# Optimization experiments

Hardware: AMD Instinct MI355X
Metric: run time of the kernel (lower is better)

## Reference

```python
import jax, jax.numpy as jnp
import numpy as np

B, S, D = 2, 2048, 2048
H, DH, DR = 16, 128, 64
DC_KV, DC_Q = 512, 1536
ROPE_BASE = 10000.0


def _rope(t):
    """Apply rotate-half RoPE over the last dim of t: [B, S, H, DR]."""
    s, dr = t.shape[1], t.shape[-1]
    inv_freq = 1.0 / (ROPE_BASE ** (jnp.arange(0, dr, 2, dtype=jnp.float32) / dr))
    ang = jnp.arange(s, dtype=jnp.float32)[:, None] * inv_freq  # [S, DR/2]
    cos = jnp.tile(jnp.cos(ang), (1, 2))[None, :, None, :]  # [1,S,1,DR]
    sin = jnp.tile(jnp.sin(ang), (1, 2))[None, :, None, :]
    t1, t2 = jnp.split(t, 2, axis=-1)
    rot = jnp.concatenate([-t2, t1], axis=-1)
    return t * cos + rot * sin


def setup_inputs() -> dict:
    key = jax.random.key(0)
    ks = jax.random.split(key, 18)
    g = lambda k, shp: (jax.random.normal(k, shp, dtype=jnp.float32) * 0.02)
    return {
        "x": jax.random.normal(ks[0], (B, S, D), dtype=jnp.float32),
        "Wkd": g(ks[1], (DC_KV, D)),   "bkd": jnp.zeros((DC_KV,), jnp.float32),
        "Wqd": g(ks[2], (DC_Q, D)),    "bqd": jnp.zeros((DC_Q,), jnp.float32),
        "Wku": g(ks[3], (H * DH, DC_KV)), "bku": jnp.zeros((H * DH,), jnp.float32),
        "Wvu": g(ks[4], (H * DH, DC_KV)), "bvu": jnp.zeros((H * DH,), jnp.float32),
        "Wqu": g(ks[5], (H * DH, DC_Q)),  "bqu": jnp.zeros((H * DH,), jnp.float32),
        "Wkr": g(ks[6], (H * DR, D)),     "bkr": jnp.zeros((H * DR,), jnp.float32),
        "Wqr": g(ks[7], (H * DR, DC_Q)),  "bqr": jnp.zeros((H * DR,), jnp.float32),
        "Wo": g(ks[8], (D, H * DH)),      "bo": jnp.zeros((D,), jnp.float32),
    }


def reference(x, Wkd, bkd, Wqd, bqd, Wku, bku, Wvu, bvu, Wqu, bqu,
              Wkr, bkr, Wqr, bqr, Wo, bo):
    b, s, _ = x.shape
    # 1. Compress to latent spaces
    kv_c = x @ Wkd.T + bkd          # [B,S,DC_KV]
    q_c = x @ Wqd.T + bqd           # [B,S,DC_Q]
    # 2-3. Up-project content / value / rope features
    k_cnt = (kv_c @ Wku.T + bku).reshape(b, s, H, DH)
    v = (kv_c @ Wvu.T + bvu).reshape(b, s, H, DH)
    q_cnt = (q_c @ Wqu.T + bqu).reshape(b, s, H, DH)
    k_r = (x @ Wkr.T + bkr).reshape(b, s, H, DR)      # keys rope from input (eq. 3)
    q_r = (q_c @ Wqr.T + bqr).reshape(b, s, H, DR)    # query rope from latent (eq. 8)
    # 5. Partial RoPE: rotate position features, concat with content
    q_full = jnp.concatenate([q_cnt, _rope(q_r)], axis=-1)  # [B,S,H,DH+DR]
    k_full = jnp.concatenate([k_cnt, _rope(k_r)], axis=-1)
    # 7. Manual causal attention (mscale = 1)
    scale = 1.0 / jnp.sqrt(jnp.float32(DH + DR))
    scores = jnp.einsum("bqhd,bkhd->bhqk", q_full, k_full) * scale
    causal = jnp.tril(jnp.ones((s, s), dtype=bool))
    scores = jnp.where(causal[None, None], scores, jnp.float32(-1e9))
    probs = jax.nn.softmax(scores, axis=-1)
    attn = jnp.einsum("bhqk,bkhd->bqhd", probs, v).reshape(b, s, H * DH)
    # 9. Output projection
    return attn @ Wo.T + bo
```

## Files before the change

### kernel.cpp

```cpp
#include <hip/hip_runtime.h>
#include <stdint.h>
#include <stddef.h>

#define BB 2
#define SS 2048
#define DD 2048
#define HH 16
#define DHH 128
#define DRR 64
#define DCKV 512
#define DCQ 1536

typedef __attribute__((ext_vector_type(8))) short short8;
typedef __attribute__((ext_vector_type(4))) short short4v;
typedef __attribute__((ext_vector_type(4))) float f32x4;
typedef unsigned int u32;

__device__ __forceinline__ short f2bf(float x) {
  unsigned u = __float_as_uint(x);
  u += 0x7fffu + ((u >> 16) & 1u);
  return (short)(u >> 16);
}
__device__ __forceinline__ float bf2f(short s) {
  return __uint_as_float(((unsigned)(unsigned short)s) << 16);
}

__device__ __forceinline__ void gl2lds16(const short* g, short* l) {
  __builtin_amdgcn_global_load_lds(
      (const __attribute__((address_space(1))) u32*)g,
      (__attribute__((address_space(3))) u32*)l, 16, 0, 0);
}

__global__ __launch_bounds__(256) void cast_bf16_kernel(const float* __restrict__ in,
                                                        short* __restrict__ out, int n4) {
  int i = blockIdx.x * 256 + threadIdx.x;
  if (i >= n4) return;
  f32x4 f = ((const f32x4*)in)[i];
  short4v o;
  o[0] = f2bf(f[0]); o[1] = f2bf(f[1]); o[2] = f2bf(f[2]); o[3] = f2bf(f[3]);
  ((short4v*)out)[i] = o;
}

__global__ __launch_bounds__(256) void concat_bias_kernel(
    const float* bkd, const float* bqd, const float* bkr,
    const float* bqu, const float* bqr, const float* bku, const float* bvu,
    float* cb1, float* cb2, float* cb3) {
  int idx = blockIdx.x * 256 + threadIdx.x;
  if (idx < 3072) {
    cb1[idx] = idx < 512 ? bkd[idx] : (idx < 2048 ? bqd[idx - 512] : bkr[idx - 2048]);
  } else if (idx < 6144) {
    int j = idx - 3072;
    cb2[j] = j < 2048 ? bqu[j] : bqr[j - 2048];
  } else if (idx < 10240) {
    int j = idx - 6144;
    cb3[j] = j < 2048 ? bku[j] : bvu[j - 2048];
  }
}

template<int MODE>
__global__ __launch_bounds__(256) void gemm_bt(const short* __restrict__ A, int lda,
                                               const short* __restrict__ Bm, int ldb,
                                               const float* __restrict__ bias,
                                               void* __restrict__ Cout, void* __restrict__ out2,
                                               int M, int N, int K) {
  __shared__ __align__(16) short sA[128 * 32];
  __shared__ __align__(16) short sB[128 * 32];
  const int tid = threadIdx.x;
  const int w = tid >> 6, L = tid & 63, quad = L >> 4, lc = L & 15;
  const int wm = w >> 1, wn = w & 1;
  const int tm = blockIdx.x * 128, tn = blockIdx.y * 128;
  const int lrow = L >> 2, lch = (L & 3) * 8;
  f32x4 acc[4][4] = {};
  const int nk = K >> 5;
  for (int kt = 0; kt < nk; ++kt) {
    const int k0 = kt << 5;
    __syncthreads();
    {
      int sub = w * 2;
      gl2lds16(A + (size_t)(tm + sub * 16 + lrow) * lda + k0 + lch, &sA[sub * 512]);
      gl2lds16(A + (size_t)(tm + sub * 16 + 16 + lrow) * lda + k0 + lch, &sA[sub * 512 + 512]);
      gl2lds16(Bm + (size_t)(tn + sub * 16 + lrow) * ldb + k0 + lch, &sB[sub * 512]);
      gl2lds16(Bm + (size_t)(tn + sub * 16 + 16 + lrow) * ldb + k0 + lch, &sB[sub * 512 + 512]);
    }
    __syncthreads();
    short8 af[4], bfr[4];
#pragma unroll
    for (int ms = 0; ms < 4; ++ms)
      af[ms] = *(const short8*)&sA[(wm * 64 + ms * 16 + lc) * 32 + quad * 8];
#pragma unroll
    for (int ns = 0; ns < 4; ++ns)
      bfr[ns] = *(const short8*)&sB[(wn * 64 + ns * 16 + lc) * 32 + quad * 8];
#pragma unroll
    for (int ms = 0; ms < 4; ++ms)
#pragma unroll
      for (int ns = 0; ns < 4; ++ns)
        acc[ms][ns] = __builtin_amdgcn_mfma_f32_16x16x32_bf16(af[ms], bfr[ns], acc[ms][ns], 0, 0, 0);
  }
#pragma unroll
  for (int ms = 0; ms < 4; ++ms) {
    int row = tm + wm * 64 + ms * 16 + quad * 4;
#pragma unroll
    for (int ns = 0; ns < 4; ++ns) {
      int col = tn + wn * 64 + ns * 16 + lc;
      float bv = bias[col];
#pragma unroll
      for (int r = 0; r < 4; ++r) {
        float vv = acc[ms][ns][r] + bv;
        int rrow = row + r;
        if (MODE == 0)      ((short*)Cout)[(size_t)rrow * N + col] = f2bf(vv);
        else if (MODE == 1) ((float*)Cout)[(size_t)rrow * N + col] = vv;
        else {
          if (col < 2048) {
            int b_ = rrow >> 11, s_ = rrow & 2047, h_ = col >> 7, d_ = col & 127;
            ((short*)Cout)[(((size_t)(b_ * HH + h_)) * SS + s_) * 192 + d_] = f2bf(vv);
          } else {
            int auxn = (MODE == 2) ? 1024 : 2048;
            ((short*)out2)[(size_t)rrow * auxn + (col - 2048)] = f2bf(vv);
          }
        }
      }
    }
  }
}

__global__ __launch_bounds__(256) void rope_kernel(const short* __restrict__ rin,
                                                   int rstride, int roff,
                                                   short* __restrict__ full) {
  int idx = blockIdx.x * 256 + threadIdx.x;
  int i = idx & 31, h = (idx >> 5) & 15, s = (idx >> 9) & 2047, b = idx >> 20;
  const short* base = rin + ((size_t)(b * SS + s)) * rstride + roff + h * DRR;
  float t1 = bf2f(base[i]), t2 = bf2f(base[i + 32]);
  float invf = expf(-9.210340371976184f * (float)i * (1.0f / 32.0f));
  float ang = (float)s * invf;
  float c = cosf(ang), sn = sinf(ang);
  short* ob = full + (((size_t)(b * HH + h)) * SS + s) * 192 + 128;
  ob[i]      = f2bf(t1 * c - t2 * sn);
  ob[i + 32] = f2bf(t1 * sn + t2 * c);
}

__global__ __launch_bounds__(256) void transpose_v_kernel(const short* __restrict__ v,
                                                          short* __restrict__ vt) {
  int idx = blockIdx.x * 256 + threadIdx.x;
  int s = idx & 2047, d = (idx >> 11) & 127, h = (idx >> 18) & 15, b = idx >> 22;
  vt[idx] = v[((size_t)(b * SS + s)) * 2048 + h * 128 + d];
}

__device__ __forceinline__ float quad_max(float v) {
  v = fmaxf(v, __shfl_xor(v, 1));
  v = fmaxf(v, __shfl_xor(v, 2));
  v = fmaxf(v, __shfl_xor(v, 4));
  v = fmaxf(v, __shfl_xor(v, 8));
  return v;
}
__device__ __forceinline__ float quad_sum(float v) {
  v += __shfl_xor(v, 1); v += __shfl_xor(v, 2);
  v += __shfl_xor(v, 4); v += __shfl_xor(v, 8);
  return v;
}

__global__ __launch_bounds__(256, 2) void mla_flash_kernel(const short* __restrict__ Qf,
                                                           const short* __restrict__ Kf,
                                                           const short* __restrict__ Vt,
                                                           float* __restrict__ Opart,
                                                           float* __restrict__ Mpart,
                                                           float* __restrict__ Lpart,
                                                           short* __restrict__ attn) {
  const int bid = blockIdx.x;
  const int g = (bid & 7) * 160 + (bid >> 3);
  const int bh = g / 40, xc = g - bh * 40;
  int qt, c;
  if (xc < 4)       { qt = xc;                 c = 0; }
  else if (xc < 12) { qt = 4 + ((xc - 4) >> 1);  c = (xc - 4) & 1; }
  else if (xc < 24) { qt = 8 + (xc - 12) / 3;    c = (xc - 12) % 3; }
  else              { qt = 12 + ((xc - 24) >> 2); c = (xc - 24) & 3; }
  const int k4 = c * 4;
  const int kend = (k4 + 4 < qt + 1) ? k4 + 4 : qt + 1;
  const int nc = (qt + 4) >> 2;
  const int slot = bh * 40 + xc;

  const int h = bh & 15, b = bh >> 4;
  const int tid = threadIdx.x, w = tid >> 6, L = tid & 63, quad = L >> 4, lc = L & 15;
  __shared__ __align__(16) short sK[6 * 128 * 32];
  short* Pf = sK;

  const short* Qb = Qf + ((size_t)bh) * SS * 192;
  const short* Kb = Kf + ((size_t)bh) * SS * 192;
  const short* Vb = Vt + ((size_t)bh) * DHH * SS;

  const int qrow0 = qt * 128 + w * 32;
  short8 qa[2][6];
#pragma unroll
  for (int ms = 0; ms < 2; ++ms)
#pragma unroll
    for (int kk = 0; kk < 6; ++kk)
      qa[ms][kk] = *(const short8*)(Qb + (size_t)(qrow0 + ms * 16 + lc) * 192 + kk * 32 + quad * 8);

  f32x4 O[2][8] = {};
  float mrow[2][4], lrow[2][4];
#pragma unroll
  for (int ms = 0; ms < 2; ++ms)
#pragma unroll
    for (int r = 0; r < 4; ++r) { mrow[ms][r] = -1e30f; lrow[ms][r] = 0.f; }

  for (int kt = k4; kt < kend; ++kt) {
    __syncthreads();
#pragma unroll
    for (int i = 0; i < 12; ++i) {
      int idx = i * 256 + tid;
      int seg = idx >> 9, rem = idx & 511, row = rem >> 2, q = rem & 3;
      short8 v = *(const short8*)(Kb + (size_t)(kt * 128 + row) * 192 + seg * 32 + q * 8);
      int slot2 = row * 4 + (q ^ ((row >> 1) & 3));
      *(short8*)&sK[(seg * 512 + slot2) * 8] = v;
    }
    __syncthreads();
    f32x4 sc[2][8] = {};
#pragma unroll
    for (int kk = 0; kk < 6; ++kk)
#pragma unroll
      for (int ns = 0; ns < 8; ++ns) {
        int rr = ns * 16 + lc;
        short8 kb = *(const short8*)&sK[(kk * 512 + rr * 4 + (quad ^ ((rr >> 1) & 3))) * 8];
        sc[0][ns] = __builtin_amdgcn_mfma_f32_16x16x32_bf16(qa[0][kk], kb, sc[0][ns], 0, 0, 0);
        sc[1][ns] = __builtin_amdgcn_mfma_f32_16x16x32_bf16(qa[1][kk], kb, sc[1][ns], 0, 0, 0);
      }
    const float scale = 0.07216878364870322f;
    const bool diag = (kt == qt);
#pragma unroll
    for (int ms = 0; ms < 2; ++ms)
#pragma unroll
      for (int ns = 0; ns < 8; ++ns)
#pragma unroll
        for (int r = 0; r < 4; ++r) {
          float vv = sc[ms][ns][r] * scale;
          if (diag && (ns * 16 + lc > w * 32 + ms * 16 + quad * 4 + r)) vv = -1e30f;
          sc[ms][ns][r] = vv;
        }
#pragma unroll
    for (int ms = 0; ms < 2; ++ms)
#pragma unroll
      for (int r = 0; r < 4; ++r) {
        float mx = sc[ms][0][r];
#pragma unroll
        for (int ns = 1; ns < 8; ++ns) mx = fmaxf(mx, sc[ms][ns][r]);
        mx = quad_max(mx);
        float mnew = fmaxf(mrow[ms][r], mx);
        float alpha = __expf(mrow[ms][r] - mnew);
        mrow[ms][r] = mnew;
        float ps = 0.f;
#pragma unroll
        for (int ns = 0; ns < 8; ++ns) {
          float p = __expf(sc[ms][ns][r] - mnew);
          sc[ms][ns][r] = p;
          ps += p;
        }
        ps = quad_sum(ps);
        lrow[ms][r] = lrow[ms][r] * alpha + ps;
#pragma unroll
        for (int n = 0; n < 8; ++n) O[ms][n][r] *= alpha;
      }
    __syncthreads();
#pragma unroll
    for (int ms = 0; ms < 2; ++ms)
#pragma unroll
      for (int ns = 0; ns < 8; ++ns)
#pragma unroll
        for (int r = 0; r < 4; ++r)
          Pf[(w * 32 + ms * 16 + quad * 4 + r) * 136 + ns * 16 + lc] = f2bf(sc[ms][ns][r]);
#pragma unroll
    for (int kk2 = 0; kk2 < 4; ++kk2) {
      short8 pa[2];
      pa[0] = *(const short8*)&Pf[(w * 32 + lc) * 136 + kk2 * 32 + quad * 8];
      pa[1] = *(const short8*)&Pf[(w * 32 + 16 + lc) * 136 + kk2 * 32 + quad * 8];
      short8 vb[8];
#pragma unroll
      for (int n = 0; n < 8; ++n)
        vb[n] = *(const short8*)(Vb + (size_t)(n * 16 + lc) * SS + kt * 128 + kk2 * 32 + quad * 8);
#pragma unroll
      for (int ms = 0; ms < 2; ++ms)
#pragma unroll
        for (int n = 0; n < 8; ++n)
          O[ms][n] = __builtin_amdgcn_mfma_f32_16x16x32_bf16(pa[ms], vb[n], O[ms][n], 0, 0, 0);
    }
  }
  if (nc == 1) {
#pragma unroll
    for (int ms = 0; ms < 2; ++ms)
#pragma unroll
      for (int r = 0; r < 4; ++r) {
        float inv = 1.0f / lrow[ms][r];
        int srow = qt * 128 + w * 32 + ms * 16 + quad * 4 + r;
        short* dst = attn + ((size_t)b * SS + srow) * 2048 + h * 128;
#pragma unroll
        for (int n = 0; n < 8; ++n)
          dst[n * 16 + lc] = f2bf(O[ms][n][r] * inv);
      }
  } else {
    float* Ob = Opart + (size_t)slot * 16384;
#pragma unroll
    for (int ms = 0; ms < 2; ++ms)
#pragma unroll
      for (int r = 0; r < 4; ++r) {
        int row = w * 32 + ms * 16 + quad * 4 + r;
#pragma unroll
        for (int n = 0; n < 8; ++n)
          Ob[(size_t)row * 128 + n * 16 + lc] = O[ms][n][r];
      }
    if (lc == 0) {
#pragma unroll
      for (int ms = 0; ms < 2; ++ms)
#pragma unroll
        for (int r = 0; r < 4; ++r) {
          int row = w * 32 + ms * 16 + quad * 4 + r;
          Mpart[slot * 128 + row] = mrow[ms][r];
          Lpart[slot * 128 + row] = lrow[ms][r];
        }
    }
  }
}

__global__ __launch_bounds__(256) void combine_kernel(const float* __restrict__ Op,
                                                      const float* __restrict__ Mp,
                                                      const float* __restrict__ Lp,
                                                      short* __restrict__ attn) {
  int idx = blockIdx.x * 256 + threadIdx.x;
  int col = idx & 127;
  int r = (idx >> 7) & 127;
  int t = idx >> 14;
  int bh = t / 12, qt = (t - bh * 12) + 4;
  int nc = (qt + 4) >> 2;
  int cbase;
  if (qt < 8)       cbase = 4 + 2 * (qt - 4);
  else if (qt < 12) cbase = 12 + 3 * (qt - 8);
  else              cbase = 24 + 4 * (qt - 12);
  int slot0 = bh * 40 + cbase;
  float mc[4];
#pragma unroll
  for (int cc = 0; cc < 4; ++cc)
    mc[cc] = (cc < nc) ? Mp[(size_t)(slot0 + cc) * 128 + r] : -1e30f;
  float M = fmaxf(fmaxf(mc[0], mc[1]), fmaxf(mc[2], mc[3]));
  float den = 0.f, acc = 0.f;
#pragma unroll
  for (int cc = 0; cc < 4; ++cc) {
    if (cc < nc) {
      float e = __expf(mc[cc] - M);
      den += e * Lp[(size_t)(slot0 + cc) * 128 + r];
      acc += e * Op[(size_t)(slot0 + cc) * 16384 + (size_t)r * 128 + col];
    }
  }
  int b = bh >> 4, hh = bh & 15;
  int srow = qt * 128 + r;
  attn[((size_t)b * SS + srow) * 2048 + hh * 128 + col] = f2bf(acc / den);
}

extern "C" void kernel_launch(void* const* d_in, const int* in_sizes, int n_in,
                              void* d_out, int out_size, void* d_ws, size_t ws_size,
                              hipStream_t stream) {
  const float* x   = (const float*)d_in[0];
  const float* Wkd = (const float*)d_in[1];
  const float* bkd = (const float*)d_in[2];
  const float* Wqd = (const float*)d_in[3];
  const float* bqd = (const float*)d_in[4];
  const float* Wku = (const float*)d_in[5];
  const float* bku = (const float*)d_in[6];
  const float* Wvu = (const float*)d_in[7];
  const float* bvu = (const float*)d_in[8];
  const float* Wqu = (const float*)d_in[9];
  const float* bqu = (const float*)d_in[10];
  const float* Wkr = (const float*)d_in[11];
  const float* bkr = (const float*)d_in[12];
  const float* Wqr = (const float*)d_in[13];
  const float* bqr = (const float*)d_in[14];
  const float* Wo  = (const float*)d_in[15];
  const float* bo  = (const float*)d_in[16];

  char* ws = (char*)d_ws;
  size_t off = 0;
  auto alloc = [&](size_t elems, size_t esz) -> void* {
    void* p = (void*)(ws + off);
    off += elems * esz;
    off = (off + 255) & ~(size_t)255;
    return p;
  };
  const int MS = BB * SS;
  short* xb    = (short*)alloc((size_t)MS * DD, 2);
  short* cbuf  = (short*)alloc((size_t)MS * 3072, 2);
  short* qrbuf = (short*)alloc((size_t)MS * 1024, 2);
  short* vbuf  = (short*)alloc((size_t)MS * 2048, 2);
  short* w1    = (short*)alloc((size_t)3072 * 2048, 2);
  short* w2    = (short*)alloc((size_t)3072 * 1536, 2);
  short* w3    = (short*)alloc((size_t)4096 * 512, 2);
  short* wob   = (short*)alloc((size_t)2048 * 2048, 2);
  float* cb1   = (float*)alloc(3072, 4);
  float* cb2   = (float*)alloc(3072, 4);
  float* cb3   = (float*)alloc(4096, 4);
  short* qfull = (short*)alloc((size_t)BB * HH * SS * 192, 2);
  short* kfull = (short*)alloc((size_t)BB * HH * SS * 192, 2);
  short* vt    = (short*)alloc((size_t)BB * HH * DHH * SS, 2);
  short* attn  = (short*)alloc((size_t)MS * 2048, 2);
  if (off > ws_size) return;

  float* Opart = (float*)ws;
  float* Mpart = (float*)(ws + (size_t)1280 * 16384 * 4);
  float* Lpart = (float*)(ws + (size_t)1280 * 16384 * 4 + (size_t)1280 * 128 * 4);

  auto cast = [&](const float* src, short* dst, size_t n) {
    int n4 = (int)(n >> 2);
    cast_bf16_kernel<<<dim3((unsigned)((n4 + 255) / 256)), dim3(256), 0, stream>>>(src, dst, n4);
  };
  cast(x,   xb, (size_t)MS * DD);
  cast(Wkd, w1,                          (size_t)512 * 2048);
  cast(Wqd, w1 + (size_t)512 * 2048,     (size_t)1536 * 2048);
  cast(Wkr, w1 + (size_t)2048 * 2048,    (size_t)1024 * 2048);
  cast(Wqu, w2,                          (size_t)2048 * 1536);
  cast(Wqr, w2 + (size_t)2048 * 1536,    (size_t)1024 * 1536);
  cast(Wku, w3,                          (size_t)2048 * 512);
  cast(Wvu, w3 + (size_t)2048 * 512,     (size_t)2048 * 512);
  cast(Wo,  wob,                         (size_t)2048 * 2048);
  concat_bias_kernel<<<dim3(40), dim3(256), 0, stream>>>(bkd, bqd, bkr, bqu, bqr, bku, bvu,
                                                         cb1, cb2, cb3);

  dim3 blk(256);
  gemm_bt<0><<<dim3(32, 24), blk, 0, stream>>>(xb, DD, w1, DD, cb1, cbuf, nullptr,
                                               MS, 3072, DD);
  gemm_bt<2><<<dim3(32, 24), blk, 0, stream>>>(cbuf + 512, 3072, w2, DCQ, cb2, qfull, qrbuf,
                                               MS, 3072, DCQ);
  gemm_bt<3><<<dim3(32, 32), blk, 0, stream>>>(cbuf, 3072, w3, DCKV, cb3, kfull, vbuf,
                                               MS, 4096, DCKV);

  rope_kernel<<<dim3(BB * SS * HH * 32 / 256), blk, 0, stream>>>(qrbuf, 1024, 0, qfull);
  rope_kernel<<<dim3(BB * SS * HH * 32 / 256), blk, 0, stream>>>(cbuf, 3072, 2048, kfull);
  transpose_v_kernel<<<dim3(BB * HH * DHH * SS / 256), blk, 0, stream>>>(vbuf, vt);

  mla_flash_kernel<<<dim3(1280), blk, 0, stream>>>(qfull, kfull, vt, Opart, Mpart, Lpart, attn);
  combine_kernel<<<dim3(24576), blk, 0, stream>>>(Opart, Mpart, Lpart, attn);

  gemm_bt<1><<<dim3(32, 16), blk, 0, stream>>>(attn, DD, wob, DD, bo, d_out, nullptr,
                                               MS, DD, DD);
}
```

Baseline: 631.4 us.

## Halve flash-attention query tile to 64 rows and fuse V transpose into GEMM epilogue

The attention kernel now processes 64 query rows per block (16 per wave) instead of 128, doubling the grid to 2560 blocks with a reworked split-K schedule and combine indexing, and raises the launch-bounds occupancy hint to 3. The V up-projection GEMM epilogue writes V directly in transposed [b,h,d,s] layout with packed 4-element stores, removing the separate transpose kernel and its intermediate buffer. The smaller tile aims for more parallelism and occupancy, but each K tile loaded into shared memory is now reused by half as many query rows, which increases K/V traffic.

```diff
diff --git a/kernel.cpp b/kernel.cpp
--- a/kernel.cpp
+++ b/kernel.cpp
@@ -103,19 +103,27 @@
     for (int ns = 0; ns < 4; ++ns) {
       int col = tn + wn * 64 + ns * 16 + lc;
       float bv = bias[col];
-#pragma unroll
-      for (int r = 0; r < 4; ++r) {
-        float vv = acc[ms][ns][r] + bv;
-        int rrow = row + r;
-        if (MODE == 0)      ((short*)Cout)[(size_t)rrow * N + col] = f2bf(vv);
-        else if (MODE == 1) ((float*)Cout)[(size_t)rrow * N + col] = vv;
-        else {
-          if (col < 2048) {
-            int b_ = rrow >> 11, s_ = rrow & 2047, h_ = col >> 7, d_ = col & 127;
-            ((short*)Cout)[(((size_t)(b_ * HH + h_)) * SS + s_) * 192 + d_] = f2bf(vv);
-          } else {
-            int auxn = (MODE == 2) ? 1024 : 2048;
-            ((short*)out2)[(size_t)rrow * auxn + (col - 2048)] = f2bf(vv);
+      if (MODE == 3 && col >= 2048) {
+        int j = col - 2048, h_ = j >> 7, dh = j & 127;
+        int b_ = row >> 11, s0 = row & 2047;
+        short4v pk;
+#pragma unroll
+        for (int r = 0; r < 4; ++r) pk[r] = f2bf(acc[ms][ns][r] + bv);
+        *(short4v*)((short*)out2 + (((size_t)(b_ * HH + h_)) * DHH + dh) * SS + s0) = pk;
+      } else {
+#pragma unroll
+        for (int r = 0; r < 4; ++r) {
+          float vv = acc[ms][ns][r] + bv;
+          int rrow = row + r;
+          if (MODE == 0)      ((short*)Cout)[(size_t)rrow * N + col] = f2bf(vv);
+          else if (MODE == 1) ((float*)Cout)[(size_t)rrow * N + col] = vv;
+          else {
+            if (col < 2048) {
+              int b_ = rrow >> 11, s_ = rrow & 2047, h_ = col >> 7, d_ = col & 127;
+              ((short*)Cout)[(((size_t)(b_ * HH + h_)) * SS + s_) * 192 + d_] = f2bf(vv);
+            } else {
+              ((short*)out2)[(size_t)rrow * 1024 + (col - 2048)] = f2bf(vv);
+            }
           }
         }
       }
@@ -138,13 +146,6 @@
   ob[i + 32] = f2bf(t1 * sn + t2 * c);
 }
 
-__global__ __launch_bounds__(256) void transpose_v_kernel(const short* __restrict__ v,
-                                                          short* __restrict__ vt) {
-  int idx = blockIdx.x * 256 + threadIdx.x;
-  int s = idx & 2047, d = (idx >> 11) & 127, h = (idx >> 18) & 15, b = idx >> 22;
-  vt[idx] = v[((size_t)(b * SS + s)) * 2048 + h * 128 + d];
-}
-
 __device__ __forceinline__ float quad_max(float v) {
   v = fmaxf(v, __shfl_xor(v, 1));
   v = fmaxf(v, __shfl_xor(v, 2));
@@ -158,7 +159,7 @@
   return v;
 }
 
-__global__ __launch_bounds__(256, 2) void mla_flash_kernel(const short* __restrict__ Qf,
+__global__ __launch_bounds__(256, 3) void mla_flash_kernel(const short* __restrict__ Qf,
                                                            const short* __restrict__ Kf,
                                                            const short* __restrict__ Vt,
                                                            float* __restrict__ Opart,
@@ -166,17 +167,21 @@
                                                            float* __restrict__ Lpart,
                                                            short* __restrict__ attn) {
   const int bid = blockIdx.x;
-  const int g = (bid & 7) * 160 + (bid >> 3);
-  const int bh = g / 40, xc = g - bh * 40;
-  int qt, c;
-  if (xc < 4)       { qt = xc;                 c = 0; }
-  else if (xc < 12) { qt = 4 + ((xc - 4) >> 1);  c = (xc - 4) & 1; }
-  else if (xc < 24) { qt = 8 + (xc - 12) / 3;    c = (xc - 12) % 3; }
-  else              { qt = 12 + ((xc - 24) >> 2); c = (xc - 24) & 3; }
+  const int g = (bid & 7) * 320 + (bid >> 3);
+  const int bh = g / 80, xc = g - bh * 80;
+  int qt64, c;
+  if (xc < 8)       { qt64 = xc; c = 0; }
+  else if (xc < 24) { int u = xc - 8;  int t = 4 + (u >> 2);  int rem = u & 3;
+                      qt64 = 2 * t + (rem >> 1); c = rem & 1; }
+  else if (xc < 48) { int u = xc - 24; int t = 8 + u / 6;     int rem = u % 6;
+                      qt64 = 2 * t + (rem >= 3 ? 1 : 0); c = rem >= 3 ? rem - 3 : rem; }
+  else              { int u = xc - 48; int t = 12 + (u >> 3); int rem = u & 7;
+                      qt64 = 2 * t + (rem >> 2); c = rem & 3; }
+  const int ktmax = (qt64 >> 1) + 1;
   const int k4 = c * 4;
-  const int kend = (k4 + 4 < qt + 1) ? k4 + 4 : qt + 1;
-  const int nc = (qt + 4) >> 2;
-  const int slot = bh * 40 + xc;
+  const int kend = (k4 + 4 < ktmax) ? k4 + 4 : ktmax;
+  const int nc = (ktmax + 3) >> 2;
+  const int slot = bh * 80 + xc;
 
   const int h = bh & 15, b = bh >> 4;
   const int tid = threadIdx.x, w = tid >> 6, L = tid & 63, quad = L >> 4, lc = L & 15;
@@ -187,20 +192,16 @@
   const short* Kb = Kf + ((size_t)bh) * SS * 192;
   const short* Vb = Vt + ((size_t)bh) * DHH * SS;
 
-  const int qrow0 = qt * 128 + w * 32;
-  short8 qa[2][6];
-#pragma unroll
-  for (int ms = 0; ms < 2; ++ms)
-#pragma unroll
-    for (int kk = 0; kk < 6; ++kk)
-      qa[ms][kk] = *(const short8*)(Qb + (size_t)(qrow0 + ms * 16 + lc) * 192 + kk * 32 + quad * 8);
-
-  f32x4 O[2][8] = {};
-  float mrow[2][4], lrow[2][4];
-#pragma unroll
-  for (int ms = 0; ms < 2; ++ms)
-#pragma unroll
-    for (int r = 0; r < 4; ++r) { mrow[ms][r] = -1e30f; lrow[ms][r] = 0.f; }
+  const int qrow0 = qt64 * 64 + w * 16;
+  short8 qa[6];
+#pragma unroll
+  for (int kk = 0; kk < 6; ++kk)
+    qa[kk] = *(const short8*)(Qb + (size_t)(qrow0 + lc) * 192 + kk * 32 + quad * 8);
+
+  f32x4 O[8] = {};
+  float mrow[4], lrow[4];
+#pragma unroll
+  for (int r = 0; r < 4; ++r) { mrow[r] = -1e30f; lrow[r] = 0.f; }
 
   for (int kt = k4; kt < kend; ++kt) {
     __syncthreads();
@@ -213,107 +214,90 @@
       *(short8*)&sK[(seg * 512 + slot2) * 8] = v;
     }
     __syncthreads();
-    f32x4 sc[2][8] = {};
+    f32x4 sc[8] = {};
 #pragma unroll
     for (int kk = 0; kk < 6; ++kk)
 #pragma unroll
       for (int ns = 0; ns < 8; ++ns) {
         int rr = ns * 16 + lc;
         short8 kb = *(const short8*)&sK[(kk * 512 + rr * 4 + (quad ^ ((rr >> 1) & 3))) * 8];
-        sc[0][ns] = __builtin_amdgcn_mfma_f32_16x16x32_bf16(qa[0][kk], kb, sc[0][ns], 0, 0, 0);
-        sc[1][ns] = __builtin_amdgcn_mfma_f32_16x16x32_bf16(qa[1][kk], kb, sc[1][ns], 0, 0, 0);
+        sc[ns] = __builtin_amdgcn_mfma_f32_16x16x32_bf16(qa[kk], kb, sc[ns], 0, 0, 0);
       }
     const float scale = 0.07216878364870322f;
-    const bool diag = (kt == qt);
-#pragma unroll
-    for (int ms = 0; ms < 2; ++ms)
-#pragma unroll
-      for (int ns = 0; ns < 8; ++ns)
-#pragma unroll
-        for (int r = 0; r < 4; ++r) {
-          float vv = sc[ms][ns][r] * scale;
-          if (diag && (ns * 16 + lc > w * 32 + ms * 16 + quad * 4 + r)) vv = -1e30f;
-          sc[ms][ns][r] = vv;
-        }
-#pragma unroll
-    for (int ms = 0; ms < 2; ++ms)
+    const bool diag = (kt == ktmax - 1) && (kt * 128 + 128 > qt64 * 64);
+#pragma unroll
+    for (int ns = 0; ns < 8; ++ns)
 #pragma unroll
       for (int r = 0; r < 4; ++r) {
-        float mx = sc[ms][0][r];
-#pragma unroll
-        for (int ns = 1; ns < 8; ++ns) mx = fmaxf(mx, sc[ms][ns][r]);
-        mx = quad_max(mx);
-        float mnew = fmaxf(mrow[ms][r], mx);
-        float alpha = __expf(mrow[ms][r] - mnew);
-        mrow[ms][r] = mnew;
-        float ps = 0.f;
-#pragma unroll
-        for (int ns = 0; ns < 8; ++ns) {
-          float p = __expf(sc[ms][ns][r] - mnew);
-          sc[ms][ns][r] = p;
-          ps += p;
-        }
-        ps = quad_sum(ps);
-        lrow[ms][r] = lrow[ms][r] * alpha + ps;
-#pragma unroll
-        for (int n = 0; n < 8; ++n) O[ms][n][r] *= alpha;
+        float vv = sc[ns][r] * scale;
+        if (diag && (kt * 128 + ns * 16 + lc > qrow0 + quad * 4 + r)) vv = -1e30f;
+        sc[ns][r] = vv;
       }
+#pragma unroll
+    for (int r = 0; r < 4; ++r) {
+      float mx = sc[0][r];
+#pragma unroll
+      for (int ns = 1; ns < 8; ++ns) mx = fmaxf(mx, sc[ns][r]);
+      mx = quad_max(mx);
+      float mnew = fmaxf(mrow[r], mx);
+      float alpha = __expf(mrow[r] - mnew);
+      mrow[r] = mnew;
+      float ps = 0.f;
+#pragma unroll
+      for (int ns = 0; ns < 8; ++ns) {
+        float p = __expf(sc[ns][r] - mnew);
+        sc[ns][r] = p;
+        ps += p;
+      }
+      ps = quad_sum(ps);
+      lrow[r] = lrow[r] * alpha + ps;
+#pragma unroll
+      for (int n = 0; n < 8; ++n) O[n][r] *= alpha;
+    }
     __syncthreads();
 #pragma unroll
-    for (int ms = 0; ms < 2; ++ms)
-#pragma unroll
-      for (int ns = 0; ns < 8; ++ns)
-#pragma unroll
-        for (int r = 0; r < 4; ++r)
-          Pf[(w * 32 + ms * 16 + quad * 4 + r) * 136 + ns * 16 + lc] = f2bf(sc[ms][ns][r]);
+    for (int ns = 0; ns < 8; ++ns)
+#pragma unroll
+      for (int r = 0; r < 4; ++r)
+        Pf[(w * 16 + quad * 4 + r) * 136 + ns * 16 + lc] = f2bf(sc[ns][r]);
 #pragma unroll
     for (int kk2 = 0; kk2 < 4; ++kk2) {
-      short8 pa[2];
-      pa[0] = *(const short8*)&Pf[(w * 32 + lc) * 136 + kk2 * 32 + quad * 8];
-      pa[1] = *(const short8*)&Pf[(w * 32 + 16 + lc) * 136 + kk2 * 32 + quad * 8];
+      short8 pa = *(const short8*)&Pf[(w * 16 + lc) * 136 + kk2 * 32 + quad * 8];
       short8 vb[8];
 #pragma unroll
       for (int n = 0; n < 8; ++n)
         vb[n] = *(const short8*)(Vb + (size_t)(n * 16 + lc) * SS + kt * 128 + kk2 * 32 + quad * 8);
 #pragma unroll
-      for (int ms = 0; ms < 2; ++ms)
-#pragma unroll
-        for (int n = 0; n < 8; ++n)
-          O[ms][n] = __builtin_amdgcn_mfma_f32_16x16x32_bf16(pa[ms], vb[n], O[ms][n], 0, 0, 0);
+      for (int n = 0; n < 8; ++n)
+        O[n] = __builtin_amdgcn_mfma_f32_16x16x32_bf16(pa, vb[n], O[n], 0, 0, 0);
     }
   }
   if (nc == 1) {
 #pragma unroll
-    for (int ms = 0; ms < 2; ++ms)
+    for (int r = 0; r < 4; ++r) {
+      float inv = 1.0f / lrow[r];
+      int srow = qt64 * 64 + w * 16 + quad * 4 + r;
+      short* dst = attn + ((size_t)b * SS + srow) * 2048 + h * 128;
+#pragma unroll
+      for (int n = 0; n < 8; ++n)
+        dst[n * 16 + lc] = f2bf(O[n][r] * inv);
+    }
+  } else {
+    float* Ob = Opart + (size_t)slot * 8192;
+#pragma unroll
+    for (int r = 0; r < 4; ++r) {
+      int row = w * 16 + quad * 4 + r;
+#pragma unroll
+      for (int n = 0; n < 8; ++n)
+        Ob[(size_t)row * 128 + n * 16 + lc] = O[n][r];
+    }
+    if (lc == 0) {
 #pragma unroll
       for (int r = 0; r < 4; ++r) {
-        float inv = 1.0f / lrow[ms][r];
-        int srow = qt * 128 + w * 32 + ms * 16 + quad * 4 + r;
-        short* dst = attn + ((size_t)b * SS + srow) * 2048 + h * 128;
-#pragma unroll
-        for (int n = 0; n < 8; ++n)
-          dst[n * 16 + lc] = f2bf(O[ms][n][r] * inv);
+        int row = w * 16 + quad * 4 + r;
+        Mpart[slot * 64 + row] = mrow[r];
+        Lpart[slot * 64 + row] = lrow[r];
       }
-  } else {
-    float* Ob = Opart + (size_t)slot * 16384;
-#pragma unroll
-    for (int ms = 0; ms < 2; ++ms)
-#pragma unroll
-      for (int r = 0; r < 4; ++r) {
-        int row = w * 32 + ms * 16 + quad * 4 + r;
-#pragma unroll
-        for (int n = 0; n < 8; ++n)
-          Ob[(size_t)row * 128 + n * 16 + lc] = O[ms][n][r];
-      }
-    if (lc == 0) {
-#pragma unroll
-      for (int ms = 0; ms < 2; ++ms)
-#pragma unroll
-        for (int r = 0; r < 4; ++r) {
-          int row = w * 32 + ms * 16 + quad * 4 + r;
-          Mpart[slot * 128 + row] = mrow[ms][r];
-          Lpart[slot * 128 + row] = lrow[ms][r];
-        }
     }
   }
 }
@@ -324,31 +308,32 @@
                                                       short* __restrict__ attn) {
   int idx = blockIdx.x * 256 + threadIdx.x;
   int col = idx & 127;
-  int r = (idx >> 7) & 127;
-  int t = idx >> 14;
-  int bh = t / 12, qt = (t - bh * 12) + 4;
-  int nc = (qt + 4) >> 2;
-  int cbase;
-  if (qt < 8)       cbase = 4 + 2 * (qt - 4);
-  else if (qt < 12) cbase = 12 + 3 * (qt - 8);
-  else              cbase = 24 + 4 * (qt - 12);
-  int slot0 = bh * 40 + cbase;
+  int r = (idx >> 7) & 63;
+  int t2 = idx >> 13;
+  int bh = t2 / 24, qt64 = (t2 - bh * 24) + 8;
+  int nc = (qt64 >> 3) + 1;
+  int t = qt64 >> 1, odd = qt64 & 1;
+  int oc, onc;
+  if (t < 8)       { oc = 4 + 2 * (t - 4);   onc = 2; }
+  else if (t < 12) { oc = 12 + 3 * (t - 8);  onc = 3; }
+  else             { oc = 24 + 4 * (t - 12); onc = 4; }
+  int slot0 = bh * 80 + 2 * oc + odd * onc;
   float mc[4];
 #pragma unroll
   for (int cc = 0; cc < 4; ++cc)
-    mc[cc] = (cc < nc) ? Mp[(size_t)(slot0 + cc) * 128 + r] : -1e30f;
+    mc[cc] = (cc < nc) ? Mp[(size_t)(slot0 + cc) * 64 + r] : -1e30f;
   float M = fmaxf(fmaxf(mc[0], mc[1]), fmaxf(mc[2], mc[3]));
   float den = 0.f, acc = 0.f;
 #pragma unroll
   for (int cc = 0; cc < 4; ++cc) {
     if (cc < nc) {
       float e = __expf(mc[cc] - M);
-      den += e * Lp[(size_t)(slot0 + cc) * 128 + r];
-      acc += e * Op[(size_t)(slot0 + cc) * 16384 + (size_t)r * 128 + col];
+      den += e * Lp[(size_t)(slot0 + cc) * 64 + r];
+      acc += e * Op[(size_t)(slot0 + cc) * 8192 + (size_t)r * 128 + col];
     }
   }
   int b = bh >> 4, hh = bh & 15;
-  int srow = qt * 128 + r;
+  int srow = qt64 * 64 + r;
   attn[((size_t)b * SS + srow) * 2048 + hh * 128 + col] = f2bf(acc / den);
 }
 
@@ -400,8 +385,8 @@
   if (off > ws_size) return;
 
   float* Opart = (float*)ws;
-  float* Mpart = (float*)(ws + (size_t)1280 * 16384 * 4);
-  float* Lpart = (float*)(ws + (size_t)1280 * 16384 * 4 + (size_t)1280 * 128 * 4);
+  float* Mpart = (float*)(ws + (size_t)2560 * 8192 * 4);
+  float* Lpart = (float*)(ws + (size_t)2560 * 8192 * 4 + (size_t)2560 * 64 * 4);
 
   auto cast = [&](const float* src, short* dst, size_t n) {
     int n4 = (int)(n >> 2);
@@ -424,14 +409,13 @@
                                                MS, 3072, DD);
   gemm_bt<2><<<dim3(32, 24), blk, 0, stream>>>(cbuf + 512, 3072, w2, DCQ, cb2, qfull, qrbuf,
                                                MS, 3072, DCQ);
-  gemm_bt<3><<<dim3(32, 32), blk, 0, stream>>>(cbuf, 3072, w3, DCKV, cb3, kfull, vbuf,
+  gemm_bt<3><<<dim3(32, 32), blk, 0, stream>>>(cbuf, 3072, w3, DCKV, cb3, kfull, vt,
                                                MS, 4096, DCKV);
 
   rope_kernel<<<dim3(BB * SS * HH * 32 / 256), blk, 0, stream>>>(qrbuf, 1024, 0, qfull);
   rope_kernel<<<dim3(BB * SS * HH * 32 / 256), blk, 0, stream>>>(cbuf, 3072, 2048, kfull);
-  transpose_v_kernel<<<dim3(BB * HH * DHH * SS / 256), blk, 0, stream>>>(vbuf, vt);
-
-  mla_flash_kernel<<<dim3(1280), blk, 0, stream>>>(qfull, kfull, vt, Opart, Mpart, Lpart, attn);
+
+  mla_flash_kernel<<<dim3(2560), blk, 0, stream>>>(qfull, kfull, vt, Opart, Mpart, Lpart, attn);
   combine_kernel<<<dim3(24576), blk, 0, stream>>>(Opart, Mpart, Lpart, attn);
 
   gemm_bt<1><<<dim3(32, 16), blk, 0, stream>>>(attn, DD, wob, DD, bo, d_out, nullptr,
```

Measured after the change: 638.6 us. About the same (+1.1%).

## Fuse V transpose into GEMM epilogue and double-buffer 64-wide K tiles in flash

Applied to the files above, without the earlier changes.

The V up-projection GEMM epilogue now writes V directly in transposed [b,h,d,s] layout with packed 4-element stores, which removes the separate transpose kernel and its extra pass through memory. The flash attention kernel switches from 128-key to 64-key tiles. K for the next tile is prefetched into registers and the shared-memory K buffer is double-buffered, so each iteration needs one barrier instead of three. P gets its own XOR-swizzled shared buffer, and causal masking is computed per element rather than only on the diagonal tile. The cost is more shared memory, more loop iterations, extra registers for the prefetch, and mask arithmetic applied on every tile.

```diff
diff --git a/kernel.cpp b/kernel.cpp
--- a/kernel.cpp
+++ b/kernel.cpp
@@ -103,19 +103,27 @@
     for (int ns = 0; ns < 4; ++ns) {
       int col = tn + wn * 64 + ns * 16 + lc;
       float bv = bias[col];
-#pragma unroll
-      for (int r = 0; r < 4; ++r) {
-        float vv = acc[ms][ns][r] + bv;
-        int rrow = row + r;
-        if (MODE == 0)      ((short*)Cout)[(size_t)rrow * N + col] = f2bf(vv);
-        else if (MODE == 1) ((float*)Cout)[(size_t)rrow * N + col] = vv;
-        else {
-          if (col < 2048) {
-            int b_ = rrow >> 11, s_ = rrow & 2047, h_ = col >> 7, d_ = col & 127;
-            ((short*)Cout)[(((size_t)(b_ * HH + h_)) * SS + s_) * 192 + d_] = f2bf(vv);
-          } else {
-            int auxn = (MODE == 2) ? 1024 : 2048;
-            ((short*)out2)[(size_t)rrow * auxn + (col - 2048)] = f2bf(vv);
+      if (MODE == 3 && col >= 2048) {
+        int j = col - 2048, h_ = j >> 7, dh = j & 127;
+        int b_ = row >> 11, s0 = row & 2047;
+        short4v pk;
+#pragma unroll
+        for (int r = 0; r < 4; ++r) pk[r] = f2bf(acc[ms][ns][r] + bv);
+        *(short4v*)((short*)out2 + (((size_t)(b_ * HH + h_)) * DHH + dh) * SS + s0) = pk;
+      } else {
+#pragma unroll
+        for (int r = 0; r < 4; ++r) {
+          float vv = acc[ms][ns][r] + bv;
+          int rrow = row + r;
+          if (MODE == 0)      ((short*)Cout)[(size_t)rrow * N + col] = f2bf(vv);
+          else if (MODE == 1) ((float*)Cout)[(size_t)rrow * N + col] = vv;
+          else {
+            if (col < 2048) {
+              int b_ = rrow >> 11, s_ = rrow & 2047, h_ = col >> 7, d_ = col & 127;
+              ((short*)Cout)[(((size_t)(b_ * HH + h_)) * SS + s_) * 192 + d_] = f2bf(vv);
+            } else {
+              ((short*)out2)[(size_t)rrow * 1024 + (col - 2048)] = f2bf(vv);
+            }
           }
         }
       }
@@ -138,13 +146,6 @@
   ob[i + 32] = f2bf(t1 * sn + t2 * c);
 }
 
-__global__ __launch_bounds__(256) void transpose_v_kernel(const short* __restrict__ v,
-                                                          short* __restrict__ vt) {
-  int idx = blockIdx.x * 256 + threadIdx.x;
-  int s = idx & 2047, d = (idx >> 11) & 127, h = (idx >> 18) & 15, b = idx >> 22;
-  vt[idx] = v[((size_t)(b * SS + s)) * 2048 + h * 128 + d];
-}
-
 __device__ __forceinline__ float quad_max(float v) {
   v = fmaxf(v, __shfl_xor(v, 1));
   v = fmaxf(v, __shfl_xor(v, 2));
@@ -166,22 +167,23 @@
                                                            float* __restrict__ Lpart,
                                                            short* __restrict__ attn) {
   const int bid = blockIdx.x;
-  const int g = (bid & 7) * 160 + (bid >> 3);
-  const int bh = g / 40, xc = g - bh * 40;
+  const int g0 = (bid & 7) * 160 + (bid >> 3);
+  const int bh = g0 / 40, xc = g0 - bh * 40;
   int qt, c;
-  if (xc < 4)       { qt = xc;                 c = 0; }
+  if (xc < 4)       { qt = xc;                  c = 0; }
   else if (xc < 12) { qt = 4 + ((xc - 4) >> 1);  c = (xc - 4) & 1; }
   else if (xc < 24) { qt = 8 + (xc - 12) / 3;    c = (xc - 12) % 3; }
   else              { qt = 12 + ((xc - 24) >> 2); c = (xc - 24) & 3; }
-  const int k4 = c * 4;
-  const int kend = (k4 + 4 < qt + 1) ? k4 + 4 : qt + 1;
   const int nc = (qt + 4) >> 2;
+  const int k8 = c * 8;
+  const int klim = 2 * qt + 2;
+  const int kend = (k8 + 8 < klim) ? k8 + 8 : klim;
   const int slot = bh * 40 + xc;
 
   const int h = bh & 15, b = bh >> 4;
   const int tid = threadIdx.x, w = tid >> 6, L = tid & 63, quad = L >> 4, lc = L & 15;
-  __shared__ __align__(16) short sK[6 * 128 * 32];
-  short* Pf = sK;
+  __shared__ __align__(16) short sK[2][12288];
+  __shared__ __align__(16) short Pf[8192];
 
   const short* Qb = Qf + ((size_t)bh) * SS * 192;
   const short* Kb = Kf + ((size_t)bh) * SS * 192;
@@ -202,53 +204,57 @@
 #pragma unroll
     for (int r = 0; r < 4; ++r) { mrow[ms][r] = -1e30f; lrow[ms][r] = 0.f; }
 
-  for (int kt = k4; kt < kend; ++kt) {
+  const int srow_ = tid >> 2, sq_ = tid & 3;
+  const int sslot = srow_ * 4 + (sq_ ^ ((srow_ >> 1) & 3));
+  short8 g[6];
+#pragma unroll
+  for (int i = 0; i < 6; ++i)
+    g[i] = *(const short8*)(Kb + (size_t)(k8 * 64 + srow_) * 192 + i * 32 + sq_ * 8);
+
+  int cur = 0;
+  for (int kt = k8; kt < kend; ++kt) {
+#pragma unroll
+    for (int i = 0; i < 6; ++i)
+      *(short8*)&sK[cur][(i * 256 + sslot) * 8] = g[i];
+    if (kt + 1 < kend) {
+#pragma unroll
+      for (int i = 0; i < 6; ++i)
+        g[i] = *(const short8*)(Kb + (size_t)((kt + 1) * 64 + srow_) * 192 + i * 32 + sq_ * 8);
+    }
     __syncthreads();
-#pragma unroll
-    for (int i = 0; i < 12; ++i) {
-      int idx = i * 256 + tid;
-      int seg = idx >> 9, rem = idx & 511, row = rem >> 2, q = rem & 3;
-      short8 v = *(const short8*)(Kb + (size_t)(kt * 128 + row) * 192 + seg * 32 + q * 8);
-      int slot2 = row * 4 + (q ^ ((row >> 1) & 3));
-      *(short8*)&sK[(seg * 512 + slot2) * 8] = v;
-    }
-    __syncthreads();
-    f32x4 sc[2][8] = {};
+    f32x4 sc[2][4] = {};
 #pragma unroll
     for (int kk = 0; kk < 6; ++kk)
 #pragma unroll
-      for (int ns = 0; ns < 8; ++ns) {
+      for (int ns = 0; ns < 4; ++ns) {
         int rr = ns * 16 + lc;
-        short8 kb = *(const short8*)&sK[(kk * 512 + rr * 4 + (quad ^ ((rr >> 1) & 3))) * 8];
+        short8 kb = *(const short8*)&sK[cur][(kk * 256 + rr * 4 + (quad ^ ((rr >> 1) & 3))) * 8];
         sc[0][ns] = __builtin_amdgcn_mfma_f32_16x16x32_bf16(qa[0][kk], kb, sc[0][ns], 0, 0, 0);
         sc[1][ns] = __builtin_amdgcn_mfma_f32_16x16x32_bf16(qa[1][kk], kb, sc[1][ns], 0, 0, 0);
       }
     const float scale = 0.07216878364870322f;
-    const bool diag = (kt == qt);
 #pragma unroll
     for (int ms = 0; ms < 2; ++ms)
 #pragma unroll
-      for (int ns = 0; ns < 8; ++ns)
+      for (int ns = 0; ns < 4; ++ns)
 #pragma unroll
         for (int r = 0; r < 4; ++r) {
           float vv = sc[ms][ns][r] * scale;
-          if (diag && (ns * 16 + lc > w * 32 + ms * 16 + quad * 4 + r)) vv = -1e30f;
+          if (kt * 64 + ns * 16 + lc > qrow0 + ms * 16 + quad * 4 + r) vv = -1e30f;
           sc[ms][ns][r] = vv;
         }
 #pragma unroll
     for (int ms = 0; ms < 2; ++ms)
 #pragma unroll
       for (int r = 0; r < 4; ++r) {
-        float mx = sc[ms][0][r];
-#pragma unroll
-        for (int ns = 1; ns < 8; ++ns) mx = fmaxf(mx, sc[ms][ns][r]);
+        float mx = fmaxf(fmaxf(sc[ms][0][r], sc[ms][1][r]), fmaxf(sc[ms][2][r], sc[ms][3][r]));
         mx = quad_max(mx);
         float mnew = fmaxf(mrow[ms][r], mx);
         float alpha = __expf(mrow[ms][r] - mnew);
         mrow[ms][r] = mnew;
         float ps = 0.f;
 #pragma unroll
-        for (int ns = 0; ns < 8; ++ns) {
+        for (int ns = 0; ns < 4; ++ns) {
           float p = __expf(sc[ms][ns][r] - mnew);
           sc[ms][ns][r] = p;
           ps += p;
@@ -258,29 +264,32 @@
 #pragma unroll
         for (int n = 0; n < 8; ++n) O[ms][n][r] *= alpha;
       }
-    __syncthreads();
 #pragma unroll
     for (int ms = 0; ms < 2; ++ms)
 #pragma unroll
-      for (int ns = 0; ns < 8; ++ns)
-#pragma unroll
-        for (int r = 0; r < 4; ++r)
-          Pf[(w * 32 + ms * 16 + quad * 4 + r) * 136 + ns * 16 + lc] = f2bf(sc[ms][ns][r]);
-#pragma unroll
-    for (int kk2 = 0; kk2 < 4; ++kk2) {
-      short8 pa[2];
-      pa[0] = *(const short8*)&Pf[(w * 32 + lc) * 136 + kk2 * 32 + quad * 8];
-      pa[1] = *(const short8*)&Pf[(w * 32 + 16 + lc) * 136 + kk2 * 32 + quad * 8];
+      for (int ns = 0; ns < 4; ++ns)
+#pragma unroll
+        for (int r = 0; r < 4; ++r) {
+          int row = w * 32 + ms * 16 + quad * 4 + r;
+          int col = ns * 16 + lc;
+          Pf[row * 64 + (((col >> 3) ^ (row & 7)) << 3) + (col & 7)] = f2bf(sc[ms][ns][r]);
+        }
+#pragma unroll
+    for (int kk2 = 0; kk2 < 2; ++kk2) {
+      int r0 = w * 32 + lc, r1 = w * 32 + 16 + lc;
+      short8 pa0 = *(const short8*)&Pf[r0 * 64 + (((kk2 * 4 + quad) ^ (r0 & 7)) << 3)];
+      short8 pa1 = *(const short8*)&Pf[r1 * 64 + (((kk2 * 4 + quad) ^ (r1 & 7)) << 3)];
       short8 vb[8];
 #pragma unroll
       for (int n = 0; n < 8; ++n)
-        vb[n] = *(const short8*)(Vb + (size_t)(n * 16 + lc) * SS + kt * 128 + kk2 * 32 + quad * 8);
-#pragma unroll
-      for (int ms = 0; ms < 2; ++ms)
-#pragma unroll
-        for (int n = 0; n < 8; ++n)
-          O[ms][n] = __builtin_amdgcn_mfma_f32_16x16x32_bf16(pa[ms], vb[n], O[ms][n], 0, 0, 0);
-    }
+        vb[n] = *(const short8*)(Vb + (size_t)(n * 16 + lc) * SS + kt * 64 + kk2 * 32 + quad * 8);
+#pragma unroll
+      for (int n = 0; n < 8; ++n) {
+        O[0][n] = __builtin_amdgcn_mfma_f32_16x16x32_bf16(pa0, vb[n], O[0][n], 0, 0, 0);
+        O[1][n] = __builtin_amdgcn_mfma_f32_16x16x32_bf16(pa1, vb[n], O[1][n], 0, 0, 0);
+      }
+    }
+    cur ^= 1;
   }
   if (nc == 1) {
 #pragma unroll
@@ -424,12 +433,11 @@
                                                MS, 3072, DD);
   gemm_bt<2><<<dim3(32, 24), blk, 0, stream>>>(cbuf + 512, 3072, w2, DCQ, cb2, qfull, qrbuf,
                                                MS, 3072, DCQ);
-  gemm_bt<3><<<dim3(32, 32), blk, 0, stream>>>(cbuf, 3072, w3, DCKV, cb3, kfull, vbuf,
+  gemm_bt<3><<<dim3(32, 32), blk, 0, stream>>>(cbuf, 3072, w3, DCKV, cb3, kfull, vt,
                                                MS, 4096, DCKV);
 
   rope_kernel<<<dim3(BB * SS * HH * 32 / 256), blk, 0, stream>>>(qrbuf, 1024, 0, qfull);
   rope_kernel<<<dim3(BB * SS * HH * 32 / 256), blk, 0, stream>>>(cbuf, 3072, 2048, kfull);
-  transpose_v_kernel<<<dim3(BB * HH * DHH * SS / 256), blk, 0, stream>>>(vbuf, vt);
 
   mla_flash_kernel<<<dim3(1280), blk, 0, stream>>>(qfull, kfull, vt, Opart, Mpart, Lpart, attn);
   combine_kernel<<<dim3(24576), blk, 0, stream>>>(Opart, Mpart, Lpart, attn);
```

Result: no change. 635.5 us (+0.7%).
